# Optimization experiments

Measured on AMD Instinct MI355X. Metric: run time of the kernel, lower is better.

The kernel has to match this reference:

```python
import jax, jax.numpy as jnp
import numpy as np

WINDOW = 9
PAD = (WINDOW - 1) // 2


def setup_inputs() -> dict:
    key = jax.random.key(0)
    k1, k2 = jax.random.split(key)
    B, C, L, H = 32, 512, 4096, 8
    x = jax.random.normal(k1, (B, C, L), dtype=jnp.float32)
    W = jax.random.normal(k2, (H, C, WINDOW), dtype=jnp.float32) * (1.0 / np.sqrt(C * WINDOW))
    b = jnp.zeros((H,), dtype=jnp.float32)
    return {"x": x, "W": W, "b": b}


def reference(x, W, b):
    # conv1d: x [B,C,L], W [H,C,w] -> logits [B,H,L] (same padding, stride 1)
    logits = jax.lax.conv_general_dilated(
        x, W,
        window_strides=(1,),
        padding=[(PAD, PAD)],
        dimension_numbers=("NCH", "OIH", "NCH"),
    ) + b[None, :, None]
    # softmax over sequence length
    focus = jax.nn.softmax(logits, axis=-1)  # [B,H,L]
    # per-head weighted sum pooling over L: [B,C,H]
    pooled = jnp.einsum("bhl,bcl->bch", focus, x)
    # reduce='max' over heads -> [B,C]
    return jnp.max(pooled, axis=-1)
```

## Files before the change

### kernel.cpp

```cpp
#include <hip/hip_runtime.h>

#define B_LEN 32
#define C_LEN 512
#define L_LEN 4096
#define H_LEN 8
#define WIN 9

typedef __attribute__((ext_vector_type(8))) short short8v;
typedef __attribute__((ext_vector_type(4))) float float4v;

__device__ __forceinline__ short f2bf(float f) {
  unsigned u = __float_as_uint(f);
  unsigned r = (u + 0x7fffu + ((u >> 16) & 1u)) >> 16;
  return (short)r;
}

__global__ __launch_bounds__(256) void repack_w_bf16(
    const float* __restrict__ W, short* __restrict__ Wt)
{
  const int i = blockIdx.x * 256 + threadIdx.x;
  if (i >= WIN * 16 * C_LEN) return;
  const int c = i & 511;
  const int h = (i >> 9) & 15;
  const int w = i / (16 * C_LEN);
  const float v = (h < H_LEN) ? W[((size_t)h * C_LEN + c) * WIN + w] : 0.f;
  Wt[i] = f2bf(v);
}

#define SLICE 5760

__global__ __launch_bounds__(256, 3) void conv_mfma(
    const float* __restrict__ x, const short* __restrict__ Wt,
    float* __restrict__ part)
{
  __shared__ short xt[4 * 2 * (SLICE / 2)];
  const int t = threadIdx.x;
  const int lane = t & 63;
  const int wid = t >> 6;
  const int j15 = lane & 15;
  const int g = lane >> 4;
  const int g16 = g * 16;
  const int b = blockIdx.y;
  const int l0b = blockIdx.x * 256;
  const int wl0 = wid * 64;
  const int s = l0b + wl0 - 4;
  const float* xb = x + (size_t)b * C_LEN * L_LEN;

  char* bufA = (char*)&xt[0] + (size_t)wid * 2 * SLICE;
  char* bufB = bufA + SLICE;

  const int q = lane & 15;
  const int chigh = lane >> 4;
  const int bl = s + 4 + 4 * q;
  const int hside = lane >> 5;
  const int hc = lane & 31;
  const int hl = s + (hside ? 68 : 0);
  const bool hok = (hl >= 0) && (hl + 3 < L_LEN);
  const int hlc = hok ? hl : (hside ? (L_LEN - 4) : 0);
  const int hr = hside ? 68 : 0;
  const int hkey = hside ? 16 : 0;

  float4 L0, L1, L2, L3, L4, L5, L6, L7, LH;
  short8v wn0, wn1, wn2, wn3, wn4, wn5, wn6, wn7, wn8;
  const float4 z4 = make_float4(0.f, 0.f, 0.f, 0.f);

#define WLOAD(K)                                                               \
  {                                                                            \
    const short* Wb = Wt + (K) * 32 + j15 * 512 + 8 * g;                       \
    wn0 = *(const short8v*)(Wb);                                               \
    wn1 = *(const short8v*)(Wb + 1 * 8192);                                    \
    wn2 = *(const short8v*)(Wb + 2 * 8192);                                    \
    wn3 = *(const short8v*)(Wb + 3 * 8192);                                    \
    wn4 = *(const short8v*)(Wb + 4 * 8192);                                    \
    wn5 = *(const short8v*)(Wb + 5 * 8192);                                    \
    wn6 = *(const short8v*)(Wb + 6 * 8192);                                    \
    wn7 = *(const short8v*)(Wb + 7 * 8192);                                    \
    wn8 = *(const short8v*)(Wb + 8 * 8192);                                    \
  }

#define LOADK(K)                                                               \
  {                                                                            \
    const float* bsrc = xb + (size_t)((K) * 32 + chigh * 8) * L_LEN + bl;      \
    L0 = *(const float4*)(bsrc);                                               \
    L1 = *(const float4*)(bsrc + 1 * (size_t)L_LEN);                           \
    L2 = *(const float4*)(bsrc + 2 * (size_t)L_LEN);                           \
    L3 = *(const float4*)(bsrc + 3 * (size_t)L_LEN);                           \
    L4 = *(const float4*)(bsrc + 4 * (size_t)L_LEN);                           \
    L5 = *(const float4*)(bsrc + 5 * (size_t)L_LEN);                           \
    L6 = *(const float4*)(bsrc + 6 * (size_t)L_LEN);                           \
    L7 = *(const float4*)(bsrc + 7 * (size_t)L_LEN);                           \
    LH = *(const float4*)(xb + (size_t)((K) * 32 + hc) * L_LEN + hlc);         \
    if (!hok) LH = z4;                                                         \
  }

#define WROW(BB, E, CMP)                                                       \
  {                                                                            \
    const int r = 4 + 4 * q + (E);                                             \
    short8v v = { f2bf(L0.CMP), f2bf(L1.CMP), f2bf(L2.CMP), f2bf(L3.CMP),      \
                  f2bf(L4.CMP), f2bf(L5.CMP), f2bf(L6.CMP), f2bf(L7.CMP) };    \
    *(short8v*)((BB) + r * 80 + ((chigh * 16) ^ (((r >> 2) & 3) << 4))) = v;   \
  }

#define WRITEB(BB)                                                             \
  {                                                                            \
    WROW(BB, 0, x) WROW(BB, 1, y) WROW(BB, 2, z) WROW(BB, 3, w)                \
    *(short*)((BB) + (hr + 0) * 80 + ((hc * 2) ^ hkey)) = f2bf(LH.x);          \
    *(short*)((BB) + (hr + 1) * 80 + ((hc * 2) ^ hkey)) = f2bf(LH.y);          \
    *(short*)((BB) + (hr + 2) * 80 + ((hc * 2) ^ hkey)) = f2bf(LH.z);          \
    *(short*)((BB) + (hr + 3) * 80 + ((hc * 2) ^ hkey)) = f2bf(LH.w);          \
  }

#define MSTEP(BB, ROFF, ACC, WF)                                               \
  {                                                                            \
    const int r = rw + (ROFF);                                                 \
    short8v xf = *(const short8v*)((BB) + r * 80 + (g16 ^ (((r >> 2) & 3) << 4))); \
    ACC = __builtin_amdgcn_mfma_f32_16x16x32_bf16(WF, xf, ACC, 0, 0, 0);       \
  }

#define CSTEP(BB, W, WF)                                                       \
  {                                                                            \
    const int rw = j15 + (W);                                                  \
    MSTEP(BB, 0, acc0, WF) MSTEP(BB, 16, acc1, WF)                             \
    MSTEP(BB, 32, acc2, WF) MSTEP(BB, 48, acc3, WF)                            \
  }

#define COMPUTE(BB)                                                            \
  {                                                                            \
    __builtin_amdgcn_s_setprio(1);                                             \
    CSTEP(BB, 0, wn0) CSTEP(BB, 1, wn1) CSTEP(BB, 2, wn2)                      \
    CSTEP(BB, 3, wn3) CSTEP(BB, 4, wn4) CSTEP(BB, 5, wn5)                      \
    CSTEP(BB, 6, wn6) CSTEP(BB, 7, wn7) CSTEP(BB, 8, wn8)                      \
    __builtin_amdgcn_s_setprio(0);                                             \
  }

  float4v acc0 = {0.f, 0.f, 0.f, 0.f};
  float4v acc1 = acc0, acc2 = acc0, acc3 = acc0;

  LOADK(0)
  WRITEB(bufA)

  for (int i = 0; i < 16; i += 2) {
    WLOAD(i)
    LOADK(i + 1)
    COMPUTE(bufA)
    WRITEB(bufB)
    WLOAD(i + 1)
    if (i + 2 < 16) { LOADK(i + 2) }
    COMPUTE(bufB)
    if (i + 2 < 16) { WRITEB(bufA) }
  }

  if (lane < 32) {
    float* d = part + ((size_t)b * H_LEN + 4 * g) * L_LEN + (l0b + wl0 + j15);
#pragma unroll
    for (int r = 0; r < 4; ++r) {
      d[(size_t)r * L_LEN +  0] = acc0[r];
      d[(size_t)r * L_LEN + 16] = acc1[r];
      d[(size_t)r * L_LEN + 32] = acc2[r];
      d[(size_t)r * L_LEN + 48] = acc3[r];
    }
  }
#undef WLOAD
#undef LOADK
#undef WROW
#undef WRITEB
#undef MSTEP
#undef CSTEP
#undef COMPUTE
}

__global__ __launch_bounds__(256) void softmax_rows(
    const float* __restrict__ part, float* __restrict__ focus)
{
  __shared__ float red[256];
  const int r = blockIdx.x;
  const int t = threadIdx.x;
  float v[16];
#pragma unroll
  for (int k = 0; k < 4; ++k) {
    const int i4 = (t + 256 * k) * 4;
    float4 a = *reinterpret_cast<const float4*>(&part[(size_t)r * L_LEN + i4]);
    v[4 * k + 0] = a.x; v[4 * k + 1] = a.y; v[4 * k + 2] = a.z; v[4 * k + 3] = a.w;
  }
  float m = v[0];
#pragma unroll
  for (int k = 1; k < 16; ++k) m = fmaxf(m, v[k]);
  red[t] = m;
  __syncthreads();
  for (int s = 128; s > 0; s >>= 1) {
    if (t < s) red[t] = fmaxf(red[t], red[t + s]);
    __syncthreads();
  }
  m = red[0];
  __syncthreads();
  float sum = 0.f;
#pragma unroll
  for (int k = 0; k < 16; ++k) { v[k] = __expf(v[k] - m); sum += v[k]; }
  red[t] = sum;
  __syncthreads();
  for (int s = 128; s > 0; s >>= 1) {
    if (t < s) red[t] += red[t + s];
    __syncthreads();
  }
  const float inv = 1.f / red[0];
#pragma unroll
  for (int k = 0; k < 4; ++k) {
    const int i4 = (t + 256 * k) * 4;
    float4 a;
    a.x = v[4 * k + 0] * inv; a.y = v[4 * k + 1] * inv;
    a.z = v[4 * k + 2] * inv; a.w = v[4 * k + 3] * inv;
    *reinterpret_cast<float4*>(&focus[(size_t)r * L_LEN + i4]) = a;
  }
}

#define K3_ST 68
#define K3_NS 4

__global__ __launch_bounds__(256) void pool_partial(
    const float* __restrict__ x, const float* __restrict__ focus,
    float* __restrict__ pool2)
{
  __shared__ float xs[64 * K3_ST];
  const int t = threadIdx.x;
  const int cl = t & 63;
  const int p = t >> 6;
  const int pu = __builtin_amdgcn_readfirstlane(p);
  const int b = blockIdx.y;
  const int c0 = blockIdx.x * 64;
  const int lbeg = blockIdx.z * (L_LEN / K3_NS);
  const float* f0 = focus + ((size_t)b * H_LEN + pu) * L_LEN;
  const float* f1 = f0 + 4 * (size_t)L_LEN;
  const float* xb = x + (size_t)b * C_LEN * L_LEN;
  const int srow = t >> 4;
  const int scol = (t & 15) * 4;
  float acc0 = 0.f, acc1 = 0.f;

  for (int l0 = lbeg; l0 < lbeg + L_LEN / K3_NS; l0 += 64) {
    __syncthreads();
#pragma unroll
    for (int pass = 0; pass < 4; ++pass) {
      const int c = srow + pass * 16;
      float4 v = *reinterpret_cast<const float4*>(&xb[(size_t)(c0 + c) * L_LEN + l0 + scol]);
      *reinterpret_cast<float4*>(&xs[c * K3_ST + scol]) = v;
    }
    __syncthreads();
#pragma unroll
    for (int l4 = 0; l4 < 16; ++l4) {
      const float4 xv = *reinterpret_cast<const float4*>(&xs[cl * K3_ST + 4 * l4]);
      const int li = l0 + 4 * l4;
      acc0 = fmaf(xv.x, f0[li + 0], acc0);
      acc0 = fmaf(xv.y, f0[li + 1], acc0);
      acc0 = fmaf(xv.z, f0[li + 2], acc0);
      acc0 = fmaf(xv.w, f0[li + 3], acc0);
      acc1 = fmaf(xv.x, f1[li + 0], acc1);
      acc1 = fmaf(xv.y, f1[li + 1], acc1);
      acc1 = fmaf(xv.z, f1[li + 2], acc1);
      acc1 = fmaf(xv.w, f1[li + 3], acc1);
    }
  }
  float* dst = pool2 + (((size_t)blockIdx.z * B_LEN + b) * C_LEN + c0 + cl) * H_LEN;
  dst[p] = acc0;
  dst[p + 4] = acc1;
}

__global__ __launch_bounds__(256) void pool_reduce(
    const float* __restrict__ pool2, float* __restrict__ out)
{
  const int i = blockIdx.x * 256 + threadIdx.x;
  float s[H_LEN];
#pragma unroll
  for (int h = 0; h < H_LEN; ++h) s[h] = 0.f;
  for (int ls = 0; ls < K3_NS; ++ls) {
    const float* src = pool2 + ((size_t)ls * B_LEN * C_LEN + i) * H_LEN;
    float4 a = *reinterpret_cast<const float4*>(src);
    float4 b4 = *reinterpret_cast<const float4*>(src + 4);
    s[0] += a.x; s[1] += a.y; s[2] += a.z; s[3] += a.w;
    s[4] += b4.x; s[5] += b4.y; s[6] += b4.z; s[7] += b4.w;
  }
  float m = s[0];
#pragma unroll
  for (int h = 1; h < H_LEN; ++h) m = fmaxf(m, s[h]);
  out[i] = m;
}

extern "C" void kernel_launch(void* const* d_in, const int* in_sizes, int n_in,
                              void* d_out, int out_size, void* d_ws, size_t ws_size,
                              hipStream_t stream)
{
  const float* x = (const float*)d_in[0];
  const float* W = (const float*)d_in[1];
  float* out = (float*)d_out;
  float* ws = (float*)d_ws;

  const size_t PART = (size_t)B_LEN * H_LEN * L_LEN;
  const size_t POOL2N = (size_t)K3_NS * B_LEN * C_LEN * H_LEN;

  float* part = ws;
  float* focus = ws + PART;
  float* pool2 = focus + PART;
  short* Wt = (short*)(pool2 + POOL2N);

  hipLaunchKernelGGL(repack_w_bf16, dim3((WIN * 16 * C_LEN + 255) / 256), dim3(256), 0,
                     stream, W, Wt);
  hipLaunchKernelGGL(conv_mfma, dim3(L_LEN / 256, B_LEN), dim3(256), 0,
                     stream, x, Wt, part);
  hipLaunchKernelGGL(softmax_rows, dim3(B_LEN * H_LEN), dim3(256), 0,
                     stream, part, focus);
  hipLaunchKernelGGL(pool_partial, dim3(C_LEN / 64, B_LEN, K3_NS), dim3(256), 0,
                     stream, x, focus, pool2);
  hipLaunchKernelGGL(pool_reduce, dim3((B_LEN * C_LEN) / 256), dim3(256), 0,
                     stream, pool2, out);
}
```

Baseline: 138.9 us.

## Pack even and odd conv taps into MFMA M dimension to halve MFMA count

The 16-row MFMA M dimension previously held 8 heads plus 8 zero-padded rows. It now carries the 8 heads at even taps in rows 0-7 and the same heads at odd taps in rows 8-15. This cuts the per-chunk MFMA steps from 9 to 5 and the weight fragment loads to match. The odd-tap results land in a separate partHi buffer shifted by one position, and softmax adds partLo and partHi. A special block in the repack kernel computes the missing last-position boundary term, at the cost of an extra workspace buffer and extra reads in softmax.

Result: slower. 207.5 us (+49.4%).

```diff
diff --git a/kernel.cpp b/kernel.cpp
--- a/kernel.cpp
+++ b/kernel.cpp
@@ -16,14 +16,30 @@
 }
 
 __global__ __launch_bounds__(256) void repack_w_bf16(
-    const float* __restrict__ W, short* __restrict__ Wt)
-{
+    const float* __restrict__ W, const float* __restrict__ x,
+    short* __restrict__ Wt, float* __restrict__ partHi)
+{
+  if (blockIdx.x == 160) {
+    const int t = threadIdx.x;
+    const int b = t >> 3, h = t & 7;
+    const float* xc = x + (size_t)b * C_LEN * L_LEN;
+    float s1 = 0.f, s3 = 0.f;
+    for (int c = 0; c < C_LEN; ++c) {
+      const float x92 = xc[(size_t)c * L_LEN + 4092];
+      const float x94 = xc[(size_t)c * L_LEN + 4094];
+      s1 = fmaf(W[((size_t)h * C_LEN + c) * WIN + 1], x92, s1);
+      s3 = fmaf(W[((size_t)h * C_LEN + c) * WIN + 3], x94, s3);
+    }
+    partHi[((size_t)b * H_LEN + h) * L_LEN + 4095] = s1 + s3;
+    return;
+  }
   const int i = blockIdx.x * 256 + threadIdx.x;
-  if (i >= WIN * 16 * C_LEN) return;
   const int c = i & 511;
-  const int h = (i >> 9) & 15;
-  const int w = i / (16 * C_LEN);
-  const float v = (h < H_LEN) ? W[((size_t)h * C_LEN + c) * WIN + w] : 0.f;
+  const int m = (i >> 9) & 15;
+  const int p = i / (16 * C_LEN);
+  float v = 0.f;
+  if (m < 8) v = W[((size_t)m * C_LEN + c) * WIN + 2 * p];
+  else if (2 * p + 1 < WIN) v = W[((size_t)(m - 8) * C_LEN + c) * WIN + 2 * p + 1];
   Wt[i] = f2bf(v);
 }
 
@@ -31,7 +47,7 @@
 
 __global__ __launch_bounds__(256, 3) void conv_mfma(
     const float* __restrict__ x, const short* __restrict__ Wt,
-    float* __restrict__ part)
+    float* __restrict__ partLo, float* __restrict__ partHi)
 {
   __shared__ short xt[4 * 2 * (SLICE / 2)];
   const int t = threadIdx.x;
@@ -61,7 +77,7 @@
   const int hkey = hside ? 16 : 0;
 
   float4 L0, L1, L2, L3, L4, L5, L6, L7, LH;
-  short8v wn0, wn1, wn2, wn3, wn4, wn5, wn6, wn7, wn8;
+  short8v wn0, wn1, wn2, wn3, wn4;
   const float4 z4 = make_float4(0.f, 0.f, 0.f, 0.f);
 
 #define WLOAD(K)                                                               \
@@ -72,10 +88,6 @@
     wn2 = *(const short8v*)(Wb + 2 * 8192);                                    \
     wn3 = *(const short8v*)(Wb + 3 * 8192);                                    \
     wn4 = *(const short8v*)(Wb + 4 * 8192);                                    \
-    wn5 = *(const short8v*)(Wb + 5 * 8192);                                    \
-    wn6 = *(const short8v*)(Wb + 6 * 8192);                                    \
-    wn7 = *(const short8v*)(Wb + 7 * 8192);                                    \
-    wn8 = *(const short8v*)(Wb + 8 * 8192);                                    \
   }
 
 #define LOADK(K)                                                               \
@@ -126,11 +138,8 @@
 
 #define COMPUTE(BB)                                                            \
   {                                                                            \
-    __builtin_amdgcn_s_setprio(1);                                             \
-    CSTEP(BB, 0, wn0) CSTEP(BB, 1, wn1) CSTEP(BB, 2, wn2)                      \
-    CSTEP(BB, 3, wn3) CSTEP(BB, 4, wn4) CSTEP(BB, 5, wn5)                      \
-    CSTEP(BB, 6, wn6) CSTEP(BB, 7, wn7) CSTEP(BB, 8, wn8)                      \
-    __builtin_amdgcn_s_setprio(0);                                             \
+    CSTEP(BB, 0, wn0) CSTEP(BB, 2, wn1) CSTEP(BB, 4, wn2)                      \
+    CSTEP(BB, 6, wn3) CSTEP(BB, 8, wn4)                                        \
   }
 
   float4v acc0 = {0.f, 0.f, 0.f, 0.f};
@@ -150,11 +159,22 @@
     if (i + 2 < 16) { WRITEB(bufA) }
   }
 
-  if (lane < 32) {
-    float* d = part + ((size_t)b * H_LEN + 4 * g) * L_LEN + (l0b + wl0 + j15);
+  const int lbase = l0b + wl0 + j15;
+  if (g < 2) {
+    float* d = partLo + ((size_t)b * H_LEN + 4 * g) * L_LEN + lbase;
 #pragma unroll
     for (int r = 0; r < 4; ++r) {
       d[(size_t)r * L_LEN +  0] = acc0[r];
+      d[(size_t)r * L_LEN + 16] = acc1[r];
+      d[(size_t)r * L_LEN + 32] = acc2[r];
+      d[(size_t)r * L_LEN + 48] = acc3[r];
+    }
+  } else {
+    const int lh = lbase - 1;
+    float* d = partHi + ((size_t)b * H_LEN + 4 * (g - 2)) * L_LEN + lh;
+#pragma unroll
+    for (int r = 0; r < 4; ++r) {
+      if (lh >= 0) d[(size_t)r * L_LEN + 0] = acc0[r];
       d[(size_t)r * L_LEN + 16] = acc1[r];
       d[(size_t)r * L_LEN + 32] = acc2[r];
       d[(size_t)r * L_LEN + 48] = acc3[r];
@@ -170,7 +190,8 @@
 }
 
 __global__ __launch_bounds__(256) void softmax_rows(
-    const float* __restrict__ part, float* __restrict__ focus)
+    const float* __restrict__ partLo, const float* __restrict__ partHi,
+    float* __restrict__ focus)
 {
   __shared__ float red[256];
   const int r = blockIdx.x;
@@ -179,8 +200,10 @@
 #pragma unroll
   for (int k = 0; k < 4; ++k) {
     const int i4 = (t + 256 * k) * 4;
-    float4 a = *reinterpret_cast<const float4*>(&part[(size_t)r * L_LEN + i4]);
-    v[4 * k + 0] = a.x; v[4 * k + 1] = a.y; v[4 * k + 2] = a.z; v[4 * k + 3] = a.w;
+    float4 a = *reinterpret_cast<const float4*>(&partLo[(size_t)r * L_LEN + i4]);
+    float4 c = *reinterpret_cast<const float4*>(&partHi[(size_t)r * L_LEN + i4]);
+    v[4 * k + 0] = a.x + c.x; v[4 * k + 1] = a.y + c.y;
+    v[4 * k + 2] = a.z + c.z; v[4 * k + 3] = a.w + c.w;
   }
   float m = v[0];
 #pragma unroll
@@ -295,17 +318,18 @@
   const size_t PART = (size_t)B_LEN * H_LEN * L_LEN;
   const size_t POOL2N = (size_t)K3_NS * B_LEN * C_LEN * H_LEN;
 
-  float* part = ws;
-  float* focus = ws + PART;
+  float* partLo = ws;
+  float* partHi = ws + PART;
+  float* focus = ws + 2 * PART;
   float* pool2 = focus + PART;
-  short* Wt = (short*)(pool2 + POOL2N);
-
-  hipLaunchKernelGGL(repack_w_bf16, dim3((WIN * 16 * C_LEN + 255) / 256), dim3(256), 0,
-                     stream, W, Wt);
+  short* Wt2 = (short*)(pool2 + POOL2N);
+
+  hipLaunchKernelGGL(repack_w_bf16, dim3(161), dim3(256), 0,
+                     stream, W, x, Wt2, partHi);
   hipLaunchKernelGGL(conv_mfma, dim3(L_LEN / 256, B_LEN), dim3(256), 0,
-                     stream, x, Wt, part);
+                     stream, x, Wt2, partLo, partHi);
   hipLaunchKernelGGL(softmax_rows, dim3(B_LEN * H_LEN), dim3(256), 0,
-                     stream, part, focus);
+                     stream, partLo, partHi, focus);
   hipLaunchKernelGGL(pool_partial, dim3(C_LEN / 64, B_LEN, K3_NS), dim3(256), 0,
                      stream, x, focus, pool2);
   hipLaunchKernelGGL(pool_reduce, dim3((B_LEN * C_LEN) / 256), dim3(256), 0,
```
